# Kernel optimization log

Measured on AMD Instinct MI355X. Metric: run time of the kernel, lower is better.

## Reference

```python
import jax, jax.numpy as jnp
import numpy as np

N_NODES = 50000
N_EDGES = 800000
D = 128


def _gcn_norm(edge_index, edge_weights, n_nodes):
    # PyG gcn_norm with add_self_loops=True, fill_value=1.0
    src = jnp.concatenate([edge_index[0], jnp.arange(n_nodes)])
    dst = jnp.concatenate([edge_index[1], jnp.arange(n_nodes)])
    w = jnp.concatenate([edge_weights, jnp.ones((n_nodes,), edge_weights.dtype)])
    deg = jax.ops.segment_sum(w, dst, num_segments=n_nodes)
    dinv = jnp.where(deg > 0, jax.lax.rsqrt(deg), 0.0)
    norm = dinv[src] * w * dinv[dst]  # [E + N]
    return src, dst, norm


def _gcn_conv(x, src, dst, norm, W, b, n_nodes):
    h = x @ W                                   # [N, F_out]
    msg = h[src] * norm[:, None]                # gather + scale, [E+N, F_out]
    out = jax.ops.segment_sum(msg, dst, num_segments=n_nodes)
    return out + b


def setup_inputs() -> dict:
    key = jax.random.key(0)
    ks = jax.random.split(key, 12)
    s = 1.0 / np.sqrt(D)
    return {
        "x": jax.random.normal(ks[0], (N_NODES, D), jnp.float32),
        "edge_index": jax.random.randint(ks[1], (2, N_EDGES), 0, N_NODES, jnp.int64),
        "edge_weights": jax.random.uniform(ks[2], (N_EDGES,), jnp.float32),
        "W1": jax.random.normal(ks[3], (D, D), jnp.float32) * s,
        "b1": jnp.zeros((D,), jnp.float32),
        "W2": jax.random.normal(ks[4], (D, D), jnp.float32) * s,
        "b2": jnp.zeros((D,), jnp.float32),
        "W3": jax.random.normal(ks[5], (D, D), jnp.float32) * s,
        "b3": jnp.zeros((D,), jnp.float32),
        "Wl": jax.random.normal(ks[6], (D, D), jnp.float32) * s,
        "bl": jnp.zeros((D,), jnp.float32),
    }


def reference(x, edge_index, edge_weights, W1, b1, W2, b2, W3, b3, Wl, bl):
    n = x.shape[0]
    src, dst, norm = _gcn_norm(edge_index, edge_weights, n)
    h = _gcn_conv(x, src, dst, norm, W1, b1, n)
    h = jax.nn.relu(h)
    h = _gcn_conv(h, src, dst, norm, W2, b2, n)
    h = jax.nn.relu(h)
    h = _gcn_conv(h, src, dst, norm, W3, b3, n)
    # final 'linear' activation entry == nn.Linear(out_size, out_size)
    return h @ Wl + bl
```

## Files before the change

### kernel.cpp

```cpp
#include <hip/hip_runtime.h>
#include <hip/hip_fp16.h>


#define D 128
#define CNT64_STRIDE 8
#define SLOTS 64

typedef __attribute__((ext_vector_type(8))) _Float16 half8;
typedef __attribute__((ext_vector_type(4))) float floatx4;

template <bool A_IS_F32>
__device__ __forceinline__ void gemm_body(int bid, const void* Aptr,
                                          const float* W, const float* bias,
                                          float* C32, __half* C16, int N) {
    __shared__ _Float16 Wl[128][136];
    int tid = threadIdx.x;

#pragma unroll
    for (int j = 0; j < 32; j++) {
        int e = tid + j * 512;
        Wl[e & 127][e >> 7] = (_Float16)W[e];
    }
    __syncthreads();

    int wave = tid >> 6, lane = tid & 63;
    int m = lane & 15, q = lane >> 4;
    int R0 = bid * 128 + wave * 16;

    const float*  A32p = (const float*)Aptr;
    const __half* A16p = (const __half*)Aptr;

    floatx4 acc[8];
#pragma unroll
    for (int ct = 0; ct < 8; ct++) acc[ct] = (floatx4){0.f, 0.f, 0.f, 0.f};

    int arow = R0 + m;
    bool rok = arow < N;

#pragma unroll
    for (int kk = 0; kk < 4; kk++) {
        half8 a = {0, 0, 0, 0, 0, 0, 0, 0};
        if (rok) {
            if (A_IS_F32) {
                const float* p = &A32p[(size_t)arow * 128 + kk * 32 + q * 8];
                float4 f0 = *(const float4*)p;
                float4 f1 = *(const float4*)(p + 4);
                a[0] = (_Float16)f0.x; a[1] = (_Float16)f0.y;
                a[2] = (_Float16)f0.z; a[3] = (_Float16)f0.w;
                a[4] = (_Float16)f1.x; a[5] = (_Float16)f1.y;
                a[6] = (_Float16)f1.z; a[7] = (_Float16)f1.w;
            } else {
                a = *(const half8*)&A16p[(size_t)arow * 128 + kk * 32 + q * 8];
            }
        }
#pragma unroll
        for (int ct = 0; ct < 8; ct++) {
            half8 b = *(const half8*)&Wl[ct * 16 + m][kk * 32 + q * 8];
            acc[ct] = __builtin_amdgcn_mfma_f32_16x16x32_f16(a, b, acc[ct], 0, 0, 0);
        }
    }

#pragma unroll
    for (int r = 0; r < 4; r++) {
        int row = R0 + q * 4 + r;
        if (row >= N) continue;
#pragma unroll
        for (int ct = 0; ct < 8; ct++) {
            int col = ct * 16 + m;
            float v = acc[ct][r];
            if (C16) C16[(size_t)row * 128 + col] = __float2half_rn(v);
            if (C32) C32[(size_t)row * 128 + col] = v + bias[col];
        }
    }
}

template <bool A_IS_F32>
__global__ __launch_bounds__(512) void k_gemm_mfma(const void* __restrict__ Aptr,
                                                   const float* __restrict__ W,
                                                   const float* __restrict__ bias,
                                                   float* __restrict__ C32,
                                                   __half* __restrict__ C16, int N) {
    gemm_body<A_IS_F32>(blockIdx.x, Aptr, W, bias, C32, C16, N);
}

__global__ __launch_bounds__(512) void k_build_gemm1(const float* __restrict__ x,
                                                     const float* __restrict__ W1,
                                                     __half* __restrict__ y16,
                                                     const int* __restrict__ dst,
                                                     const float* __restrict__ w,
                                                     unsigned long long* __restrict__ cnt8,
                                                     int* __restrict__ loc,
                                                     int N, int E, int gg, int ggp) {
    int b = (int)blockIdx.x;
    if (b < gg) {
        gemm_body<true>(b, x, W1, nullptr, nullptr, y16, N);
        return;
    }
    if (b < ggp) return;
    int e = (b - ggp) * 512 + threadIdx.x;
    if (e < E) {
        int d = dst[e];
        unsigned int wq = __float2uint_rn(w[e] * 32767.0f);
        unsigned long long old =
            atomicAdd(&cnt8[(size_t)d * CNT64_STRIDE], (1ull << 32) | (unsigned long long)wq);
        loc[e] = (int)(old >> 32);
    }
}

__global__ __launch_bounds__(256) void k_fill(const int* __restrict__ ei,
                                              const float* __restrict__ w,
                                              const unsigned int* __restrict__ wsum32,
                                              const int* __restrict__ loc,
                                              unsigned int* __restrict__ ev, int E) {
    int e = blockIdx.x * 256 + threadIdx.x;
    if (e < E) {
        int s = ei[e];
        int d = ei[E + e];
        float dvs = rsqrtf(1.0f + (float)wsum32[(size_t)s * 16] * (1.0f / 32767.0f));
        float dvd = rsqrtf(1.0f + (float)wsum32[(size_t)d * 16] * (1.0f / 32767.0f));
        float val = w[e] * dvs * dvd;
        unsigned int wq = __float2uint_rn(val * 32767.0f);
        ev[(size_t)d * SLOTS + loc[e]] = (wq << 17) | (unsigned int)s;
    }
}

__device__ __forceinline__ void fma8(float acc[8], float v, uint4 q) {
    union { uint4 uu; __half2 h2[4]; } U; U.uu = q;
    float2 f0 = __half22float2(U.h2[0]);
    float2 f1 = __half22float2(U.h2[1]);
    float2 f2 = __half22float2(U.h2[2]);
    float2 f3 = __half22float2(U.h2[3]);
    acc[0] = fmaf(v, f0.x, acc[0]); acc[1] = fmaf(v, f0.y, acc[1]);
    acc[2] = fmaf(v, f1.x, acc[2]); acc[3] = fmaf(v, f1.y, acc[3]);
    acc[4] = fmaf(v, f2.x, acc[4]); acc[5] = fmaf(v, f2.y, acc[5]);
    acc[6] = fmaf(v, f3.x, acc[6]); acc[7] = fmaf(v, f3.y, acc[7]);
}

__global__ __launch_bounds__(256) void k_agg(const __half* __restrict__ y16,
                                             const unsigned long long* __restrict__ cnt8,
                                             const unsigned int* __restrict__ ev,
                                             const float* __restrict__ bias,
                                             __half* __restrict__ out16,
                                             int N, int relu) {
    int wave = threadIdx.x >> 6;
    int lane = threadIdx.x & 63;
    int h  = lane >> 5;
    int r5 = lane & 31;
    int g  = r5 >> 4;
    int sl = r5 & 15;

    int i = blockIdx.x * 8 + wave * 2 + h;
    if (i >= N) return;

    const unsigned int* evp = ev + (size_t)i * SLOTS;

    unsigned long long pk = cnt8[(size_t)i * CNT64_STRIDE];
    uint4 ea = *(const uint4*)&evp[g * 8];
    uint4 eb = *(const uint4*)&evp[g * 8 + 4];

    int cnt = min((int)(pk >> 32), SLOTS);
    float di = rsqrtf(1.0f + (float)(unsigned int)pk * (1.0f / 32767.0f));

    float acc[8];
#pragma unroll
    for (int j = 0; j < 8; j++) acc[j] = 0.f;

    {
        unsigned int p[8] = {ea.x, ea.y, ea.z, ea.w, eb.x, eb.y, eb.z, eb.w};
        float v[8]; uint4 q4[8];
#pragma unroll
        for (int u = 0; u < 8; u++) {
            bool ok = (g * 8 + u) < cnt;
            v[u] = ok ? (float)(p[u] >> 17) * (1.0f / 32767.0f) : 0.0f;
            int s = min((int)(p[u] & 0x1FFFFu), N - 1);
            q4[u] = *(const uint4*)&y16[(size_t)s * D + sl * 8];
        }
#pragma unroll
        for (int u = 0; u < 8; u++) fma8(acc, v[u], q4[u]);
    }

    for (int base = 16; base < cnt; base += 16) {
        uint4 ta = *(const uint4*)&evp[base + g * 8];
        uint4 tb = *(const uint4*)&evp[base + g * 8 + 4];
        unsigned int p[8] = {ta.x, ta.y, ta.z, ta.w, tb.x, tb.y, tb.z, tb.w};
        float v[8]; uint4 q4[8];
#pragma unroll
        for (int u = 0; u < 8; u++) {
            bool ok = (base + g * 8 + u) < cnt;
            v[u] = ok ? (float)(p[u] >> 17) * (1.0f / 32767.0f) : 0.0f;
            int s = min((int)(p[u] & 0x1FFFFu), N - 1);
            q4[u] = *(const uint4*)&y16[(size_t)s * D + sl * 8];
        }
#pragma unroll
        for (int u = 0; u < 8; u++) fma8(acc, v[u], q4[u]);
    }

#pragma unroll
    for (int j = 0; j < 8; j++) acc[j] += __shfl_xor(acc[j], 16, 64);

    if (g == 0) {
        float di2 = di * di;
        union { uint4 u; __half2 h2[4]; } S;
        S.u = *(const uint4*)&y16[(size_t)i * D + sl * 8];
        float2 s0 = __half22float2(S.h2[0]);
        float2 s1 = __half22float2(S.h2[1]);
        float2 s2 = __half22float2(S.h2[2]);
        float2 s3 = __half22float2(S.h2[3]);
        float4 b0 = *(const float4*)&bias[sl * 8];
        float4 b1 = *(const float4*)&bias[sl * 8 + 4];
        float o[8];
        o[0] = b0.x + acc[0] + di2 * s0.x;
        o[1] = b0.y + acc[1] + di2 * s0.y;
        o[2] = b0.z + acc[2] + di2 * s1.x;
        o[3] = b0.w + acc[3] + di2 * s1.y;
        o[4] = b1.x + acc[4] + di2 * s2.x;
        o[5] = b1.y + acc[5] + di2 * s2.y;
        o[6] = b1.z + acc[6] + di2 * s3.x;
        o[7] = b1.w + acc[7] + di2 * s3.y;
        if (relu) {
#pragma unroll
            for (int j = 0; j < 8; j++) o[j] = fmaxf(o[j], 0.f);
        }
        union { uint4 u; __half2 h2[4]; } O;
        O.h2[0] = __float22half2_rn(make_float2(o[0], o[1]));
        O.h2[1] = __float22half2_rn(make_float2(o[2], o[3]));
        O.h2[2] = __float22half2_rn(make_float2(o[4], o[5]));
        O.h2[3] = __float22half2_rn(make_float2(o[6], o[7]));
        *(uint4*)&out16[(size_t)i * D + sl * 8] = O.u;
    }
}

extern "C" void kernel_launch(void* const* d_in, const int* in_sizes, int n_in,
                              void* d_out, int out_size, void* d_ws, size_t ws_size,
                              hipStream_t stream) {
    const float* x  = (const float*)d_in[0];
    const int*   ei = (const int*)d_in[1];
    const float* ew = (const float*)d_in[2];
    const float* W1 = (const float*)d_in[3];
    const float* b1 = (const float*)d_in[4];
    const float* W2 = (const float*)d_in[5];
    const float* b2 = (const float*)d_in[6];
    const float* W3 = (const float*)d_in[7];
    const float* b3 = (const float*)d_in[8];
    const float* Wl = (const float*)d_in[9];
    const float* bl = (const float*)d_in[10];

    int N = in_sizes[0] / D;
    int E = in_sizes[2];

    char* ws = (char*)d_ws;
    size_t off = 0;
    auto alloc = [&](size_t bytes) {
        void* p = ws + off;
        off = (off + bytes + 255) & ~(size_t)255;
        return p;
    };
    unsigned long long* cnt8 = (unsigned long long*)alloc((size_t)N * 64);
    int*    loc  = (int*)alloc((size_t)E * 4);
    unsigned int* ev = (unsigned int*)alloc((size_t)N * SLOTS * 4);
    __half* yA   = (__half*)alloc((size_t)N * D * 2);
    __half* yB   = (__half*)alloc((size_t)N * D * 2);

    int nbE    = (E + 255) / 256;
    int nbE512 = (E + 511) / 512;
    int gg     = (N + 127) / 128;
    int ggp    = (gg + 7) & ~7;
    int ga     = (N + 7) / 8;

    hipMemsetAsync(cnt8, 0, (size_t)N * 64, stream);
    k_build_gemm1<<<ggp + nbE512, 512, 0, stream>>>(x, W1, yA, ei + E, ew,
                                                    cnt8, loc, N, E, gg, ggp);
    k_fill<<<nbE, 256, 0, stream>>>(ei, ew, (const unsigned int*)cnt8, loc, ev, E);

    k_agg<<<ga, 256, 0, stream>>>(yA, cnt8, ev, b1, yB, N, 1);
    k_gemm_mfma<false><<<gg, 512, 0, stream>>>(yB, W2, nullptr, nullptr, yA, N);
    k_agg<<<ga, 256, 0, stream>>>(yA, cnt8, ev, b2, yB, N, 1);
    k_gemm_mfma<false><<<gg, 512, 0, stream>>>(yB, W3, nullptr, nullptr, yA, N);
    k_agg<<<ga, 256, 0, stream>>>(yA, cnt8, ev, b3, yB, N, 0);
    k_gemm_mfma<false><<<gg, 512, 0, stream>>>(yB, Wl, bl, (float*)d_out, nullptr, N);
}
```

Measured before the change: 277.6 us.

## Split feature matrices into column halves and aggregate each half separately

The fp16 intermediate features are stored as two column-major halves ([2][N][64]) instead of row-major [N][128]. The GEMM writes and reads this layout, and the aggregation kernel assigns each block one half for 8 nodes, with the two halves interleaved across neighbouring blocks. Each gather now touches a 128-byte segment, so the gathered working set per pass is smaller and should get better cache locality. In exchange, twice as many aggregation blocks reread the edge lists, there is an extra shuffle reduction, and the edge-list buffer is padded because the wider loop stride can read past the 64 slots.

```diff
diff --git a/kernel.cpp b/kernel.cpp
--- a/kernel.cpp
+++ b/kernel.cpp
@@ -50,7 +50,8 @@
                 a[4] = (_Float16)f1.x; a[5] = (_Float16)f1.y;
                 a[6] = (_Float16)f1.z; a[7] = (_Float16)f1.w;
             } else {
-                a = *(const half8*)&A16p[(size_t)arow * 128 + kk * 32 + q * 8];
+                a = *(const half8*)&A16p[((size_t)(kk >> 1) * N + arow) * 64 +
+                                         (kk & 1) * 32 + q * 8];
             }
         }
 #pragma unroll
@@ -68,7 +69,9 @@
         for (int ct = 0; ct < 8; ct++) {
             int col = ct * 16 + m;
             float v = acc[ct][r];
-            if (C16) C16[(size_t)row * 128 + col] = __float2half_rn(v);
+            if (C16)
+                C16[((size_t)(ct >> 2) * N + row) * 64 + (ct & 3) * 16 + m] =
+                    __float2half_rn(v);
             if (C32) C32[(size_t)row * 128 + col] = v + bias[col];
         }
     }
@@ -142,21 +145,26 @@
                                              const float* __restrict__ bias,
                                              __half* __restrict__ out16,
                                              int N, int relu) {
+    int b = (int)blockIdx.x;
+    int x8 = b & 7;
+    int c  = x8 >> 2;
+    int nb = (b >> 3) * 4 + (x8 & 3);
+
     int wave = threadIdx.x >> 6;
     int lane = threadIdx.x & 63;
     int h  = lane >> 5;
     int r5 = lane & 31;
-    int g  = r5 >> 4;
-    int sl = r5 & 15;
-
-    int i = blockIdx.x * 8 + wave * 2 + h;
+    int g  = (r5 >> 3) & 3;
+    int sl = r5 & 7;
+
+    int i = nb * 8 + wave * 2 + h;
     if (i >= N) return;
 
+    const __half* ycol = y16 + (size_t)c * N * 64;
     const unsigned int* evp = ev + (size_t)i * SLOTS;
 
     unsigned long long pk = cnt8[(size_t)i * CNT64_STRIDE];
-    uint4 ea = *(const uint4*)&evp[g * 8];
-    uint4 eb = *(const uint4*)&evp[g * 8 + 4];
+    uint4 ea = *(const uint4*)&evp[g * 4];
 
     int cnt = min((int)(pk >> 32), SLOTS);
     float di = rsqrtf(1.0f + (float)(unsigned int)pk * (1.0f / 32767.0f));
@@ -166,20 +174,20 @@
     for (int j = 0; j < 8; j++) acc[j] = 0.f;
 
     {
-        unsigned int p[8] = {ea.x, ea.y, ea.z, ea.w, eb.x, eb.y, eb.z, eb.w};
-        float v[8]; uint4 q4[8];
-#pragma unroll
-        for (int u = 0; u < 8; u++) {
-            bool ok = (g * 8 + u) < cnt;
+        unsigned int p[4] = {ea.x, ea.y, ea.z, ea.w};
+        float v[4]; uint4 q4[4];
+#pragma unroll
+        for (int u = 0; u < 4; u++) {
+            bool ok = (g * 4 + u) < cnt;
             v[u] = ok ? (float)(p[u] >> 17) * (1.0f / 32767.0f) : 0.0f;
             int s = min((int)(p[u] & 0x1FFFFu), N - 1);
-            q4[u] = *(const uint4*)&y16[(size_t)s * D + sl * 8];
-        }
-#pragma unroll
-        for (int u = 0; u < 8; u++) fma8(acc, v[u], q4[u]);
-    }
-
-    for (int base = 16; base < cnt; base += 16) {
+            q4[u] = *(const uint4*)&ycol[(size_t)s * 64 + sl * 8];
+        }
+#pragma unroll
+        for (int u = 0; u < 4; u++) fma8(acc, v[u], q4[u]);
+    }
+
+    for (int base = 16; base < cnt; base += 32) {
         uint4 ta = *(const uint4*)&evp[base + g * 8];
         uint4 tb = *(const uint4*)&evp[base + g * 8 + 4];
         unsigned int p[8] = {ta.x, ta.y, ta.z, ta.w, tb.x, tb.y, tb.z, tb.w};
@@ -189,25 +197,28 @@
             bool ok = (base + g * 8 + u) < cnt;
             v[u] = ok ? (float)(p[u] >> 17) * (1.0f / 32767.0f) : 0.0f;
             int s = min((int)(p[u] & 0x1FFFFu), N - 1);
-            q4[u] = *(const uint4*)&y16[(size_t)s * D + sl * 8];
+            q4[u] = *(const uint4*)&ycol[(size_t)s * 64 + sl * 8];
         }
 #pragma unroll
         for (int u = 0; u < 8; u++) fma8(acc, v[u], q4[u]);
     }
 
 #pragma unroll
-    for (int j = 0; j < 8; j++) acc[j] += __shfl_xor(acc[j], 16, 64);
+    for (int j = 0; j < 8; j++) {
+        acc[j] += __shfl_xor(acc[j], 8, 64);
+        acc[j] += __shfl_xor(acc[j], 16, 64);
+    }
 
     if (g == 0) {
         float di2 = di * di;
         union { uint4 u; __half2 h2[4]; } S;
-        S.u = *(const uint4*)&y16[(size_t)i * D + sl * 8];
+        S.u = *(const uint4*)&ycol[(size_t)i * 64 + sl * 8];
         float2 s0 = __half22float2(S.h2[0]);
         float2 s1 = __half22float2(S.h2[1]);
         float2 s2 = __half22float2(S.h2[2]);
         float2 s3 = __half22float2(S.h2[3]);
-        float4 b0 = *(const float4*)&bias[sl * 8];
-        float4 b1 = *(const float4*)&bias[sl * 8 + 4];
+        float4 b0 = *(const float4*)&bias[c * 64 + sl * 8];
+        float4 b1 = *(const float4*)&bias[c * 64 + sl * 8 + 4];
         float o[8];
         o[0] = b0.x + acc[0] + di2 * s0.x;
         o[1] = b0.y + acc[1] + di2 * s0.y;
@@ -226,7 +237,7 @@
         O.h2[1] = __float22half2_rn(make_float2(o[2], o[3]));
         O.h2[2] = __float22half2_rn(make_float2(o[4], o[5]));
         O.h2[3] = __float22half2_rn(make_float2(o[6], o[7]));
-        *(uint4*)&out16[(size_t)i * D + sl * 8] = O.u;
+        *(uint4*)&out16[((size_t)c * N + i) * 64 + sl * 8] = O.u;
     }
 }
 
@@ -257,7 +268,7 @@
     };
     unsigned long long* cnt8 = (unsigned long long*)alloc((size_t)N * 64);
     int*    loc  = (int*)alloc((size_t)E * 4);
-    unsigned int* ev = (unsigned int*)alloc((size_t)N * SLOTS * 4);
+    unsigned int* ev = (unsigned int*)alloc((size_t)N * SLOTS * 4 + 1024);
     __half* yA   = (__half*)alloc((size_t)N * D * 2);
     __half* yB   = (__half*)alloc((size_t)N * D * 2);
 
@@ -265,7 +276,8 @@
     int nbE512 = (E + 511) / 512;
     int gg     = (N + 127) / 128;
     int ggp    = (gg + 7) & ~7;
-    int ga     = (N + 7) / 8;
+    int nb8    = (N + 7) / 8;
+    int ga     = ((nb8 + 3) / 4) * 8;
 
     hipMemsetAsync(cnt8, 0, (size_t)N * 64, stream);
     k_build_gemm1<<<ggp + nbE512, 512, 0, stream>>>(x, W1, yA, ei + E, ew,
```

Result: slower. 311.8 us (+12.3%).
